# Performance work log

Hardware: AMD Instinct MI355X
Metric: run time of the kernel (lower is better)

Reference implementation:

```python
import jax, jax.numpy as jnp
import numpy as np

B, T, C = 8, 1024, 1024
H, D = 16, 64  # num_heads, head_size

def setup_inputs() -> dict:
    key = jax.random.key(0)
    ks = jax.random.split(key, 6)
    s = C ** -0.5
    return {
        "x": jax.random.normal(ks[0], (B, T, C), dtype=jnp.float32),
        "Wq": jax.random.normal(ks[1], (H, C, D), dtype=jnp.float32) * s,
        "Wk": jax.random.normal(ks[2], (H, C, D), dtype=jnp.float32) * s,
        "Wv": jax.random.normal(ks[3], (H, C, D), dtype=jnp.float32) * s,
        "Wproj": jax.random.normal(ks[4], (H * D, C), dtype=jnp.float32) * ((H * D) ** -0.5),
        "bproj": jnp.zeros((C,), dtype=jnp.float32),
    }

def reference(x, Wq, Wk, Wv, Wproj, bproj):
    # per-head QKV projections, batched over heads via einsum (same math as looped heads)
    q = jnp.einsum('btc,hcd->bhtd', x, Wq)
    k = jnp.einsum('btc,hcd->bhtd', x, Wk)
    v = jnp.einsum('btc,hcd->bhtd', x, Wv)
    scale = D ** -0.5  # k.shape[-1]**-0.5 in original head
    scores = jnp.einsum('bhtd,bhsd->bhts', q, k) * scale  # [B,H,T,T]
    Tn = x.shape[1]
    causal = jnp.tril(jnp.ones((Tn, Tn), dtype=bool))
    scores = jnp.where(causal, scores, jnp.float32(-jnp.inf))
    att = jax.nn.softmax(scores, axis=-1)
    out = jnp.einsum('bhts,bhsd->bhtd', att, v)          # [B,H,T,D]
    out = out.transpose(0, 2, 1, 3).reshape(x.shape[0], Tn, H * D)  # concat heads
    return out @ Wproj + bproj  # dropout is identity at p=0.0
```

## Files before the change

### kernel.cpp

```cpp
#include <hip/hip_runtime.h>
#include <hip/hip_bf16.h>

#define B_ 8
#define T_ 1024
#define C_ 1024
#define H_ 16
#define D_ 64
#define QKVLD 3072

typedef short v4s __attribute__((ext_vector_type(4)));
typedef short v8s __attribute__((ext_vector_type(8)));
typedef float v4f __attribute__((ext_vector_type(4)));
typedef float v16f __attribute__((ext_vector_type(16)));

__device__ __forceinline__ unsigned short f2b(float f) {
    unsigned int u = __builtin_bit_cast(unsigned int, f);
    unsigned int lsb = (u >> 16) & 1u;
    u += 0x7fffu + lsb;
    return (unsigned short)(u >> 16);
}

__device__ __forceinline__ v4s pack4(float p0, float p1, float p2, float p3) {
    unsigned int a = (__builtin_bit_cast(unsigned int, p0) + 0x8000u) >> 16;
    unsigned int b = (__builtin_bit_cast(unsigned int, p1) + 0x8000u) & 0xFFFF0000u;
    unsigned int c = (__builtin_bit_cast(unsigned int, p2) + 0x8000u) >> 16;
    unsigned int d = (__builtin_bit_cast(unsigned int, p3) + 0x8000u) & 0xFFFF0000u;
    union { unsigned int u[2]; v4s v; } t;
    t.u[0] = a | b; t.u[1] = c | d;
    return t.v;
}

#define MFMA32(A, B, C) __builtin_amdgcn_mfma_f32_16x16x32_bf16(A, B, C, 0, 0, 0)
#define MFMA16(A, B, C) __builtin_amdgcn_mfma_f32_16x16x16bf16_1k(A, B, C, 0, 0, 0)

#define GLOAD16(gp, lp)                                                          \
    __builtin_amdgcn_global_load_lds(                                            \
        (const __attribute__((address_space(1))) unsigned int*)(gp),             \
        (__attribute__((address_space(3))) unsigned int*)(lp), 16, 0, 0)

__global__ void prep_kernel(const float* __restrict__ x, const float* __restrict__ Wq,
                            const float* __restrict__ Wk, const float* __restrict__ Wv,
                            const float* __restrict__ Wproj,
                            unsigned short* __restrict__ xb,
                            unsigned short* __restrict__ WqkvT,
                            unsigned short* __restrict__ WprojT) {
    __shared__ unsigned short t[64][65];
    int g = blockIdx.x;
    if (g < 8192) {
        int i = (g * 256 + (int)threadIdx.x) * 4;
        float4 v = *(const float4*)(x + i);
        ushort4 o;
        o.x = f2b(v.x); o.y = f2b(v.y); o.z = f2b(v.z); o.w = f2b(v.w);
        *(ushort4*)(xb + i) = o;
    } else if (g < 8192 + 768) {
        int idx = g - 8192;
        int z = idx >> 4;
        int h = z / 3, part = z % 3;
        const float* src = (part == 0 ? Wq : (part == 1 ? Wk : Wv)) + (size_t)h * C_ * D_;
        int c0 = (idx & 15) * 64;
        for (int i = threadIdx.x; i < 4096; i += 256) {
            int r = i >> 6, d = i & 63;
            t[d][r] = f2b(src[(size_t)(c0 + r) * D_ + d]);
        }
        __syncthreads();
        unsigned short* dst = WqkvT + (size_t)(part * 1024 + h * 64) * C_;
        for (int i = threadIdx.x; i < 4096; i += 256) {
            int d = i >> 6, r = i & 63;
            dst[(size_t)d * C_ + c0 + r] = t[d][r];
        }
    } else {
        int idx = g - 8960;
        int n0 = (idx & 15) * 64, k0 = (idx >> 4) * 64;
        for (int i = threadIdx.x; i < 4096; i += 256) {
            int r = i >> 6, c = i & 63;
            t[c][r] = f2b(Wproj[(size_t)(k0 + r) * C_ + n0 + c]);
        }
        __syncthreads();
        for (int i = threadIdx.x; i < 4096; i += 256) {
            int n = i >> 6, k = i & 63;
            WprojT[(size_t)(n0 + n) * 1024 + k0 + k] = t[n][k];
        }
    }
}

__global__ __launch_bounds__(256, 2) void gemm_qk(const unsigned short* __restrict__ A,
                                                  const unsigned short* __restrict__ Bt,
                                                  unsigned short* __restrict__ Cout,
                                                  int M, int N, int K, int ldc) {
    constexpr int ABUF = 256 * 32;
    constexpr int BBUF = 128 * 32;
    __shared__ unsigned short smem[2 * ABUF + 2 * BBUF];
    unsigned short* lA0 = smem;
    unsigned short* lB0 = smem + 2 * ABUF;

    int tid = threadIdx.x;
    int m0 = blockIdx.y * 256, n0 = blockIdx.x * 128;
    int lane = tid & 63, w = tid >> 6;
    int half = lane >> 5, l32 = lane & 31;
    int wm = w >> 1, wn = w & 1;

    const unsigned short* gA[4];
    int offA[4];
    #pragma unroll
    for (int j = 0; j < 4; j++) {
        int c = j * 256 + tid;
        int row = c >> 2;
        int col8 = ((c & 3) ^ ((row >> 1) & 3)) * 8;
        gA[j] = A + (size_t)(m0 + row) * K + col8;
        offA[j] = (j * 256 + w * 64) * 16;
    }
    const unsigned short* gB[2];
    int offB[2];
    #pragma unroll
    for (int j = 0; j < 2; j++) {
        int c = j * 256 + tid;
        int row = c >> 2;
        int col8 = ((c & 3) ^ ((row >> 1) & 3)) * 8;
        gB[j] = Bt + (size_t)(n0 + row) * K + col8;
        offB[j] = (j * 256 + w * 64) * 16;
    }

    int am[4], bn[2];
    #pragma unroll
    for (int mi = 0; mi < 4; mi++) am[mi] = wm * 128 + mi * 32 + l32;
    #pragma unroll
    for (int ni = 0; ni < 2; ni++) bn[ni] = wn * 64 + ni * 32 + l32;

    v16f acc[4][2];
    #pragma unroll
    for (int mi = 0; mi < 4; mi++)
        #pragma unroll
        for (int ni = 0; ni < 2; ni++)
            #pragma unroll
            for (int r = 0; r < 16; r++) acc[mi][ni][r] = 0.f;

    int ktiles = K >> 5;
    #pragma unroll
    for (int j = 0; j < 4; j++) GLOAD16(gA[j], (char*)lA0 + offA[j]);
    #pragma unroll
    for (int j = 0; j < 2; j++) GLOAD16(gB[j], (char*)lB0 + offB[j]);

    for (int it = 0; it < ktiles; it++) {
        int cur = it & 1, nxt = cur ^ 1;
        __asm__ volatile("s_waitcnt vmcnt(0)" ::: "memory");
        __asm__ volatile("s_barrier" ::: "memory");
        {
            int kn = (it + 1 < ktiles) ? (it + 1) * 32 : it * 32;
            #pragma unroll
            for (int j = 0; j < 4; j++) GLOAD16(gA[j] + kn, (char*)(lA0 + nxt * ABUF) + offA[j]);
            #pragma unroll
            for (int j = 0; j < 2; j++) GLOAD16(gB[j] + kn, (char*)(lB0 + nxt * BBUF) + offB[j]);
        }
        const unsigned short* bufA = lA0 + cur * ABUF;
        const unsigned short* bufB = lB0 + cur * BBUF;
        #pragma unroll
        for (int step = 0; step < 2; step++) {
            int g = step * 2 + half;
            v8s af[4], bf[2];
            #pragma unroll
            for (int mi = 0; mi < 4; mi++)
                af[mi] = *(const v8s*)&bufA[am[mi] * 32 + ((g ^ ((am[mi] >> 1) & 3)) * 8)];
            #pragma unroll
            for (int ni = 0; ni < 2; ni++)
                bf[ni] = *(const v8s*)&bufB[bn[ni] * 32 + ((g ^ ((bn[ni] >> 1) & 3)) * 8)];
            #pragma unroll
            for (int mi = 0; mi < 4; mi++)
                #pragma unroll
                for (int ni = 0; ni < 2; ni++)
                    acc[mi][ni] = __builtin_amdgcn_mfma_f32_32x32x16_bf16(af[mi], bf[ni], acc[mi][ni], 0, 0, 0);
        }
    }
    float scl = (n0 >= 1024) ? 0.125f : 1.0f;
    #pragma unroll
    for (int mi = 0; mi < 4; mi++) {
        #pragma unroll
        for (int ni = 0; ni < 2; ni++) {
            int col = n0 + wn * 64 + ni * 32 + l32;
            #pragma unroll
            for (int r = 0; r < 16; r++) {
                int row = m0 + wm * 128 + mi * 32 + (r & 3) + 8 * (r >> 2) + 4 * half;
                Cout[(size_t)row * ldc + col] = f2b(acc[mi][ni][r] * scl);
            }
        }
    }
}

__global__ __launch_bounds__(256, 3) void gemm_v(const unsigned short* __restrict__ A,
                                                 const unsigned short* __restrict__ Bt,
                                                 unsigned short* __restrict__ Vt,
                                                 int M, int N, int K) {
    constexpr int ABUF = 128 * 32;
    constexpr int BBUF = 128 * 32;
    __shared__ unsigned short lA[3 * ABUF];
    __shared__ unsigned short lB[3 * BBUF];

    int tid = threadIdx.x;
    int lane = tid & 63, w = tid >> 6;
    int half = lane >> 5, l32 = lane & 31;
    int wm = w >> 1, wn = w & 1;

    int g = blockIdx.x;
    int nbm = M / 128;
    int stripe = nbm >> 3;
    int xcd = g & 7, s = g >> 3;
    int m0 = (xcd * stripe + (s % stripe)) * 128;
    int n0 = (s / stripe) * 128;

    const unsigned short* gA[2];
    int offA[2];
    #pragma unroll
    for (int j = 0; j < 2; j++) {
        int c = j * 256 + tid;
        int row = c >> 2;
        int col8 = ((c & 3) ^ ((row >> 1) & 3)) * 8;
        gA[j] = A + (size_t)(m0 + row) * K + col8;
        offA[j] = (j * 256 + w * 64) * 16;
    }
    const unsigned short* gB[2];
    int offB[2];
    #pragma unroll
    for (int j = 0; j < 2; j++) {
        int c = j * 256 + tid;
        int row = c >> 2;
        int col8 = ((c & 3) ^ ((row >> 1) & 3)) * 8;
        gB[j] = Bt + (size_t)(n0 + row) * K + col8;
        offB[j] = (j * 256 + w * 64) * 16;
    }

    int am[2], bn[2];
    #pragma unroll
    for (int mi = 0; mi < 2; mi++) am[mi] = wm * 64 + mi * 32 + l32;
    #pragma unroll
    for (int ni = 0; ni < 2; ni++) bn[ni] = wn * 64 + ni * 32 + l32;

    v16f acc[2][2];
    #pragma unroll
    for (int mi = 0; mi < 2; mi++)
        #pragma unroll
        for (int ni = 0; ni < 2; ni++)
            #pragma unroll
            for (int r = 0; r < 16; r++) acc[mi][ni][r] = 0.f;

    int kt = K >> 5;
    #pragma unroll
    for (int j = 0; j < 2; j++) GLOAD16(gA[j], (char*)lA + offA[j]);
    #pragma unroll
    for (int j = 0; j < 2; j++) GLOAD16(gB[j], (char*)lB + offB[j]);
    #pragma unroll
    for (int j = 0; j < 2; j++) GLOAD16(gA[j] + 32, (char*)(lA + ABUF) + offA[j]);
    #pragma unroll
    for (int j = 0; j < 2; j++) GLOAD16(gB[j] + 32, (char*)(lB + BBUF) + offB[j]);

    int cur = 0;
    for (int it = 0; it < kt; it++) {
        int nx2 = cur + 2; if (nx2 >= 3) nx2 -= 3;
        __asm__ volatile("s_waitcnt vmcnt(4)" ::: "memory");
        __asm__ volatile("s_barrier" ::: "memory");
        {
            int kn = ((it + 2 < kt) ? it + 2 : kt - 1) << 5;
            #pragma unroll
            for (int j = 0; j < 2; j++) GLOAD16(gA[j] + kn, (char*)(lA + nx2 * ABUF) + offA[j]);
            #pragma unroll
            for (int j = 0; j < 2; j++) GLOAD16(gB[j] + kn, (char*)(lB + nx2 * BBUF) + offB[j]);
        }
        const unsigned short* bufA = lA + cur * ABUF;
        const unsigned short* bufB = lB + cur * BBUF;
        #pragma unroll
        for (int step = 0; step < 2; step++) {
            int gch = step * 2 + half;
            v8s af[2], bf[2];
            #pragma unroll
            for (int mi = 0; mi < 2; mi++)
                af[mi] = *(const v8s*)&bufA[am[mi] * 32 + ((gch ^ ((am[mi] >> 1) & 3)) * 8)];
            #pragma unroll
            for (int ni = 0; ni < 2; ni++)
                bf[ni] = *(const v8s*)&bufB[bn[ni] * 32 + ((gch ^ ((bn[ni] >> 1) & 3)) * 8)];
            #pragma unroll
            for (int mi = 0; mi < 2; mi++)
                #pragma unroll
                for (int ni = 0; ni < 2; ni++)
                    acc[mi][ni] = __builtin_amdgcn_mfma_f32_32x32x16_bf16(af[mi], bf[ni], acc[mi][ni], 0, 0, 0);
        }
        cur = cur + 1; if (cur >= 3) cur -= 3;
    }
    unsigned short* sT = lA;
    int bB = m0 >> 10;
    int t0 = m0 & 1023;
    #pragma unroll
    for (int p = 0; p < 2; p++) {
        __syncthreads();
        if (wn == p) {
            #pragma unroll
            for (int mi = 0; mi < 2; mi++)
                #pragma unroll
                for (int ni = 0; ni < 2; ni++) {
                    int cl = ni * 32 + l32;
                    #pragma unroll
                    for (int r = 0; r < 16; r++) {
                        int rowl = wm * 64 + mi * 32 + (r & 3) + 8 * (r >> 2) + 4 * half;
                        sT[cl * 136 + rowl] = f2b(acc[mi][ni][r]);
                    }
                }
        }
        __syncthreads();
        #pragma unroll
        for (int j = 0; j < 4; j++) {
            int c = j * 256 + tid;
            int cl = c >> 4, ch = c & 15;
            int vcol = n0 + p * 64 + cl;
            int hh = vcol >> 6, dd = vcol & 63;
            *(v8s*)&Vt[(((size_t)bB * 16 + hh) * 64 + dd) * T_ + t0 + ch * 8] =
                *(const v8s*)&sT[cl * 136 + ch * 8];
        }
    }
}

__global__ __launch_bounds__(256, 3) void gemm_proj(const unsigned short* __restrict__ A,
                                                    const unsigned short* __restrict__ Bt,
                                                    float* __restrict__ Cout,
                                                    const float* __restrict__ bias,
                                                    int M, int N, int K) {
    constexpr int ABUF = 128 * 32;
    constexpr int BBUF = 128 * 32;
    __shared__ unsigned short lA[3 * ABUF];
    __shared__ unsigned short lB[3 * BBUF];

    int tid = threadIdx.x;
    int lane = tid & 63, w = tid >> 6;
    int half = lane >> 5, l32 = lane & 31;
    int wm = w >> 1, wn = w & 1;

    int g = blockIdx.x;
    int nbm = M / 128;
    int stripe = nbm >> 3;
    int xcd = g & 7, s = g >> 3;
    int m0 = (xcd * stripe + (s % stripe)) * 128;
    int n0 = (s / stripe) * 128;

    const unsigned short* gA[2];
    int offA[2];
    #pragma unroll
    for (int j = 0; j < 2; j++) {
        int c = j * 256 + tid;
        int row = c >> 2;
        int col8 = ((c & 3) ^ ((row >> 1) & 3)) * 8;
        gA[j] = A + (size_t)(m0 + row) * K + col8;
        offA[j] = (j * 256 + w * 64) * 16;
    }
    const unsigned short* gB[2];
    int offB[2];
    #pragma unroll
    for (int j = 0; j < 2; j++) {
        int c = j * 256 + tid;
        int row = c >> 2;
        int col8 = ((c & 3) ^ ((row >> 1) & 3)) * 8;
        gB[j] = Bt + (size_t)(n0 + row) * K + col8;
        offB[j] = (j * 256 + w * 64) * 16;
    }

    int am[2], bn[2];
    #pragma unroll
    for (int mi = 0; mi < 2; mi++) am[mi] = wm * 64 + mi * 32 + l32;
    #pragma unroll
    for (int ni = 0; ni < 2; ni++) bn[ni] = wn * 64 + ni * 32 + l32;

    v16f acc[2][2];
    #pragma unroll
    for (int mi = 0; mi < 2; mi++)
        #pragma unroll
        for (int ni = 0; ni < 2; ni++)
            #pragma unroll
            for (int r = 0; r < 16; r++) acc[mi][ni][r] = 0.f;

    int kt = K >> 5;
    #pragma unroll
    for (int j = 0; j < 2; j++) GLOAD16(gA[j], (char*)lA + offA[j]);
    #pragma unroll
    for (int j = 0; j < 2; j++) GLOAD16(gB[j], (char*)lB + offB[j]);
    #pragma unroll
    for (int j = 0; j < 2; j++) GLOAD16(gA[j] + 32, (char*)(lA + ABUF) + offA[j]);
    #pragma unroll
    for (int j = 0; j < 2; j++) GLOAD16(gB[j] + 32, (char*)(lB + BBUF) + offB[j]);

    int cur = 0;
    for (int it = 0; it < kt; it++) {
        int nx2 = cur + 2; if (nx2 >= 3) nx2 -= 3;
        __asm__ volatile("s_waitcnt vmcnt(4)" ::: "memory");
        __asm__ volatile("s_barrier" ::: "memory");
        {
            int kn = ((it + 2 < kt) ? it + 2 : kt - 1) << 5;
            #pragma unroll
            for (int j = 0; j < 2; j++) GLOAD16(gA[j] + kn, (char*)(lA + nx2 * ABUF) + offA[j]);
            #pragma unroll
            for (int j = 0; j < 2; j++) GLOAD16(gB[j] + kn, (char*)(lB + nx2 * BBUF) + offB[j]);
        }
        const unsigned short* bufA = lA + cur * ABUF;
        const unsigned short* bufB = lB + cur * BBUF;
        #pragma unroll
        for (int step = 0; step < 2; step++) {
            int gch = step * 2 + half;
            v8s af[2], bf[2];
            #pragma unroll
            for (int mi = 0; mi < 2; mi++)
                af[mi] = *(const v8s*)&bufA[am[mi] * 32 + ((gch ^ ((am[mi] >> 1) & 3)) * 8)];
            #pragma unroll
            for (int ni = 0; ni < 2; ni++)
                bf[ni] = *(const v8s*)&bufB[bn[ni] * 32 + ((gch ^ ((bn[ni] >> 1) & 3)) * 8)];
            #pragma unroll
            for (int mi = 0; mi < 2; mi++)
                #pragma unroll
                for (int ni = 0; ni < 2; ni++)
                    acc[mi][ni] = __builtin_amdgcn_mfma_f32_32x32x16_bf16(af[mi], bf[ni], acc[mi][ni], 0, 0, 0);
        }
        cur = cur + 1; if (cur >= 3) cur -= 3;
    }
    #pragma unroll
    for (int mi = 0; mi < 2; mi++) {
        #pragma unroll
        for (int ni = 0; ni < 2; ni++) {
            int col = n0 + wn * 64 + ni * 32 + l32;
            #pragma unroll
            for (int r = 0; r < 16; r++) {
                int row = m0 + wm * 64 + mi * 32 + (r & 3) + 8 * (r >> 2) + 4 * half;
                Cout[(size_t)row * N + col] = acc[mi][ni][r] + bias[col];
            }
        }
    }
}

__global__ __launch_bounds__(256) void attn_kernel(const unsigned short* __restrict__ QKV,
                                                   const unsigned short* __restrict__ Vt,
                                                   unsigned short* __restrict__ Ob) {
    int bh = blockIdx.x;
    int qt = 15 - blockIdx.y;
    int b = bh >> 4, h = bh & 15;
    int tid = threadIdx.x, lane = tid & 63, w = tid >> 6;
    int quad = lane >> 4, l16 = lane & 15;
    int qg0 = qt * 64 + w * 16;

    __shared__ unsigned short lK[2][2][64][32];
    __shared__ unsigned short lV[2][2][64][32];

    v8s aq0, aq1;
    {
        const unsigned short* qp = QKV + (size_t)(b * T_ + qg0 + l16) * QKVLD + h * 64;
        aq0 = *(const v8s*)(qp + quad * 8);
        aq1 = *(const v8s*)(qp + 32 + quad * 8);
    }

    const unsigned short* gK[2];
    const unsigned short* gV[2];
    int ldsOff[2];
    #pragma unroll
    for (int j = 0; j < 2; j++) {
        int c = j * 256 + tid;
        int halfp = c >> 8, row = (c >> 2) & 63;
        int col8 = ((c & 3) ^ ((row >> 1) & 3)) * 8;
        gK[j] = QKV + (size_t)(b * T_ + row) * QKVLD + 1024 + h * 64 + halfp * 32 + col8;
        gV[j] = Vt + ((size_t)bh * 64 + row) * T_ + halfp * 32 + col8;
        ldsOff[j] = (j * 256 + w * 64) * 16;
    }
    int rcol = (quad ^ ((l16 >> 1) & 3)) * 8;

    v4f accO[4];
    float lsum = 0.f;
    #pragma unroll
    for (int i = 0; i < 4; i++) accO[i] = (v4f){0.f, 0.f, 0.f, 0.f};

    int ntiles = qt + 1;

    #pragma unroll
    for (int j = 0; j < 2; j++) GLOAD16(gK[j], (char*)&lK[0][0][0][0] + ldsOff[j]);
    #pragma unroll
    for (int j = 0; j < 2; j++) GLOAD16(gV[j], (char*)&lV[0][0][0][0] + ldsOff[j]);

    for (int it = 0; it < ntiles; it++) {
        int cur = it & 1, nxt = cur ^ 1;
        int s0 = it * 64;
        __asm__ volatile("s_waitcnt vmcnt(0)" ::: "memory");
        __asm__ volatile("s_barrier" ::: "memory");
        {
            int itn = (it + 1 < ntiles) ? it + 1 : it;
            size_t koff = (size_t)itn * 64 * QKVLD;
            #pragma unroll
            for (int j = 0; j < 2; j++)
                GLOAD16(gK[j] + koff, (char*)&lK[nxt][0][0][0] + ldsOff[j]);
            size_t voff = (size_t)itn * 64;
            #pragma unroll
            for (int j = 0; j < 2; j++)
                GLOAD16(gV[j] + voff, (char*)&lV[nxt][0][0][0] + ldsOff[j]);
        }
        v4f sf[4];
        #pragma unroll
        for (int nt = 0; nt < 4; nt++) {
            v8s bk0 = *(const v8s*)&lK[cur][0][nt * 16 + l16][rcol];
            v8s bk1 = *(const v8s*)&lK[cur][1][nt * 16 + l16][rcol];
            v4f a = (v4f){0.f, 0.f, 0.f, 0.f};
            a = MFMA32(bk0, aq0, a);
            a = MFMA32(bk1, aq1, a);
            sf[nt] = a;
        }
        bool diag = (it == ntiles - 1);
        int qg = qg0 + l16;
        v4s pP[4];
        #pragma unroll
        for (int nt = 0; nt < 4; nt++) {
            float p[4];
            #pragma unroll
            for (int r = 0; r < 4; r++) {
                float e = __expf(sf[nt][r]);
                if (diag) {
                    int sg = s0 + nt * 16 + quad * 4 + r;
                    e = (sg > qg) ? 0.f : e;
                }
                p[r] = e;
                lsum += e;
            }
            pP[nt] = pack4(p[0], p[1], p[2], p[3]);
        }
        #pragma unroll
        for (int kb = 0; kb < 4; kb++) {
            int sc_ = kb >> 1;
            int ccg = (kb & 1) * 2 + (quad >> 1);
            #pragma unroll
            for (int dt = 0; dt < 4; dt++) {
                int d = dt * 16 + l16;
                int ccp = ccg ^ ((l16 >> 1) & 3);
                v4s bv = *(const v4s*)&lV[cur][sc_][d][ccp * 8 + (quad & 1) * 4];
                accO[dt] = MFMA16(pP[kb], bv, accO[dt]);
            }
        }
    }
    float ls = lsum;
    ls += __shfl_xor(ls, 16, 64);
    ls += __shfl_xor(ls, 32, 64);
    #pragma unroll
    for (int r = 0; r < 4; r++) {
        float lq = __shfl(ls, quad * 4 + r, 64);
        float inv = 1.0f / lq;
        int q = qg0 + quad * 4 + r;
        #pragma unroll
        for (int dt = 0; dt < 4; dt++) {
            int d = dt * 16 + l16;
            Ob[(size_t)(b * T_ + q) * (H_ * D_) + h * 64 + d] = f2b(accO[dt][r] * inv);
        }
    }
}

extern "C" void kernel_launch(void* const* d_in, const int* in_sizes, int n_in,
                              void* d_out, int out_size, void* d_ws, size_t ws_size,
                              hipStream_t stream) {
    const float* x     = (const float*)d_in[0];
    const float* Wq    = (const float*)d_in[1];
    const float* Wk    = (const float*)d_in[2];
    const float* Wv    = (const float*)d_in[3];
    const float* Wproj = (const float*)d_in[4];
    const float* bproj = (const float*)d_in[5];
    float* out = (float*)d_out;

    char* ws = (char*)d_ws;
    unsigned short* xb     = (unsigned short*)ws;
    unsigned short* WqkvT  = (unsigned short*)(ws + 16777216);
    unsigned short* WprojT = (unsigned short*)(ws + 23068672);
    unsigned short* QKV    = (unsigned short*)(ws + 25165824);
    unsigned short* Vt     = (unsigned short*)(ws + 75497472);
    unsigned short* Ob     = (unsigned short*)(ws + 92274688);

    prep_kernel<<<dim3(9216), dim3(256), 0, stream>>>(x, Wq, Wk, Wv, Wproj, xb, WqkvT, WprojT);
    gemm_qk<<<dim3(16, 32), dim3(256), 0, stream>>>(xb, WqkvT, QKV, 8192, 2048, 1024, QKVLD);
    gemm_v<<<dim3(512), dim3(256), 0, stream>>>(xb, WqkvT + (size_t)2048 * 1024, Vt, 8192, 1024, 1024);
    attn_kernel<<<dim3(128, 16), dim3(256), 0, stream>>>(QKV, Vt, Ob);
    gemm_proj<<<dim3(512), dim3(256), 0, stream>>>(Ob, WprojT, out, bproj, 8192, 1024, 1024);
}
```

Before: 235.7 us.

## Triple-buffer gemm_qk LDS pipeline and remap blocks by XCD for locality

The QK projection GEMM goes from double to triple LDS buffering, with global loads issued two K-tiles ahead. The wait drops from vmcnt(0) to vmcnt(6), so one tile's loads stay in flight while the current tile is computed. The 2D grid becomes a 1D grid of 512 blocks remapped so that each XCD (block id mod 8) handles a contiguous group of M-row tiles, which is meant to improve L2 reuse of A tiles. LDS use grows from 48KB to 72KB per block, which can lower occupancy below the launch-bounds target of 2 blocks per CU.

After: 238.0 us. About the same (+0.9%).

```diff
diff --git a/kernel.cpp b/kernel.cpp
--- a/kernel.cpp
+++ b/kernel.cpp
@@ -89,16 +89,19 @@
                                                   int M, int N, int K, int ldc) {
     constexpr int ABUF = 256 * 32;
     constexpr int BBUF = 128 * 32;
-    __shared__ unsigned short smem[2 * ABUF + 2 * BBUF];
-    unsigned short* lA0 = smem;
-    unsigned short* lB0 = smem + 2 * ABUF;
+    __shared__ unsigned short lA[3 * ABUF];
+    __shared__ unsigned short lB[3 * BBUF];
 
     int tid = threadIdx.x;
-    int m0 = blockIdx.y * 256, n0 = blockIdx.x * 128;
     int lane = tid & 63, w = tid >> 6;
     int half = lane >> 5, l32 = lane & 31;
     int wm = w >> 1, wn = w & 1;
 
+    int g = blockIdx.x;
+    int xcd = g & 7, s = g >> 3;
+    int m0 = (xcd * 4 + (s & 3)) * 256;
+    int n0 = (s >> 2) * 128;
+
     const unsigned short* gA[4];
     int offA[4];
     #pragma unroll
@@ -134,41 +137,47 @@
             #pragma unroll
             for (int r = 0; r < 16; r++) acc[mi][ni][r] = 0.f;
 
-    int ktiles = K >> 5;
-    #pragma unroll
-    for (int j = 0; j < 4; j++) GLOAD16(gA[j], (char*)lA0 + offA[j]);
-    #pragma unroll
-    for (int j = 0; j < 2; j++) GLOAD16(gB[j], (char*)lB0 + offB[j]);
-
-    for (int it = 0; it < ktiles; it++) {
-        int cur = it & 1, nxt = cur ^ 1;
-        __asm__ volatile("s_waitcnt vmcnt(0)" ::: "memory");
+    int kt = K >> 5;
+    #pragma unroll
+    for (int j = 0; j < 4; j++) GLOAD16(gA[j], (char*)lA + offA[j]);
+    #pragma unroll
+    for (int j = 0; j < 2; j++) GLOAD16(gB[j], (char*)lB + offB[j]);
+    #pragma unroll
+    for (int j = 0; j < 4; j++) GLOAD16(gA[j] + 32, (char*)(lA + ABUF) + offA[j]);
+    #pragma unroll
+    for (int j = 0; j < 2; j++) GLOAD16(gB[j] + 32, (char*)(lB + BBUF) + offB[j]);
+
+    int cur = 0;
+    for (int it = 0; it < kt; it++) {
+        int nx2 = cur + 2; if (nx2 >= 3) nx2 -= 3;
+        __asm__ volatile("s_waitcnt vmcnt(6)" ::: "memory");
         __asm__ volatile("s_barrier" ::: "memory");
         {
-            int kn = (it + 1 < ktiles) ? (it + 1) * 32 : it * 32;
-            #pragma unroll
-            for (int j = 0; j < 4; j++) GLOAD16(gA[j] + kn, (char*)(lA0 + nxt * ABUF) + offA[j]);
-            #pragma unroll
-            for (int j = 0; j < 2; j++) GLOAD16(gB[j] + kn, (char*)(lB0 + nxt * BBUF) + offB[j]);
-        }
-        const unsigned short* bufA = lA0 + cur * ABUF;
-        const unsigned short* bufB = lB0 + cur * BBUF;
+            int kn = ((it + 2 < kt) ? it + 2 : kt - 1) << 5;
+            #pragma unroll
+            for (int j = 0; j < 4; j++) GLOAD16(gA[j] + kn, (char*)(lA + nx2 * ABUF) + offA[j]);
+            #pragma unroll
+            for (int j = 0; j < 2; j++) GLOAD16(gB[j] + kn, (char*)(lB + nx2 * BBUF) + offB[j]);
+        }
+        const unsigned short* bufA = lA + cur * ABUF;
+        const unsigned short* bufB = lB + cur * BBUF;
         #pragma unroll
         for (int step = 0; step < 2; step++) {
-            int g = step * 2 + half;
+            int gc = step * 2 + half;
             v8s af[4], bf[2];
             #pragma unroll
             for (int mi = 0; mi < 4; mi++)
-                af[mi] = *(const v8s*)&bufA[am[mi] * 32 + ((g ^ ((am[mi] >> 1) & 3)) * 8)];
+                af[mi] = *(const v8s*)&bufA[am[mi] * 32 + ((gc ^ ((am[mi] >> 1) & 3)) * 8)];
             #pragma unroll
             for (int ni = 0; ni < 2; ni++)
-                bf[ni] = *(const v8s*)&bufB[bn[ni] * 32 + ((g ^ ((bn[ni] >> 1) & 3)) * 8)];
+                bf[ni] = *(const v8s*)&bufB[bn[ni] * 32 + ((gc ^ ((bn[ni] >> 1) & 3)) * 8)];
             #pragma unroll
             for (int mi = 0; mi < 4; mi++)
                 #pragma unroll
                 for (int ni = 0; ni < 2; ni++)
                     acc[mi][ni] = __builtin_amdgcn_mfma_f32_32x32x16_bf16(af[mi], bf[ni], acc[mi][ni], 0, 0, 0);
         }
+        cur = cur + 1; if (cur >= 3) cur -= 3;
     }
     float scl = (n0 >= 1024) ? 0.125f : 1.0f;
     #pragma unroll
@@ -567,7 +576,7 @@
     unsigned short* Ob     = (unsigned short*)(ws + 92274688);
 
     prep_kernel<<<dim3(9216), dim3(256), 0, stream>>>(x, Wq, Wk, Wv, Wproj, xb, WqkvT, WprojT);
-    gemm_qk<<<dim3(16, 32), dim3(256), 0, stream>>>(xb, WqkvT, QKV, 8192, 2048, 1024, QKVLD);
+    gemm_qk<<<dim3(512), dim3(256), 0, stream>>>(xb, WqkvT, QKV, 8192, 2048, 1024, QKVLD);
     gemm_v<<<dim3(512), dim3(256), 0, stream>>>(xb, WqkvT + (size_t)2048 * 1024, Vt, 8192, 1024, 1024);
     attn_kernel<<<dim3(128, 16), dim3(256), 0, stream>>>(QKV, Vt, Ob);
     gemm_proj<<<dim3(512), dim3(256), 0, stream>>>(Ob, WprojT, out, bproj, 8192, 1024, 1024);
```

## Fuse Q/K and V projection GEMMs into one launch with branchy epilogue

Applied to the files above, without the earlier changes.

Merges the separate QK and V projection GEMM kernels into a single 256x128-tile kernel over the full 3072-column QKV weight. Blocks whose columns fall in the V range write a transposed V layout through shared memory, and the others write row-major Q/K with scaling. This removes one kernel launch and the tail between the two GEMMs, giving a single larger grid. In exchange the V part now uses the 2-wave/CU tile config instead of its tuned 3-stage 128x128 kernel, and the transpose staging needs larger shared-memory strides.

Result: no change. 235.6 us (-0.1%).

```diff
diff --git a/kernel.cpp b/kernel.cpp
--- a/kernel.cpp
+++ b/kernel.cpp
@@ -83,10 +83,11 @@
     }
 }
 
-__global__ __launch_bounds__(256, 2) void gemm_qk(const unsigned short* __restrict__ A,
-                                                  const unsigned short* __restrict__ Bt,
-                                                  unsigned short* __restrict__ Cout,
-                                                  int M, int N, int K, int ldc) {
+__global__ __launch_bounds__(256, 2) void gemm_qkv(const unsigned short* __restrict__ A,
+                                                   const unsigned short* __restrict__ Bt,
+                                                   unsigned short* __restrict__ Cout,
+                                                   unsigned short* __restrict__ Vt,
+                                                   int M, int N, int K, int ldc) {
     constexpr int ABUF = 256 * 32;
     constexpr int BBUF = 128 * 32;
     __shared__ unsigned short smem[2 * ABUF + 2 * BBUF];
@@ -155,14 +156,14 @@
         const unsigned short* bufB = lB0 + cur * BBUF;
         #pragma unroll
         for (int step = 0; step < 2; step++) {
-            int g = step * 2 + half;
+            int gc = step * 2 + half;
             v8s af[4], bf[2];
             #pragma unroll
             for (int mi = 0; mi < 4; mi++)
-                af[mi] = *(const v8s*)&bufA[am[mi] * 32 + ((g ^ ((am[mi] >> 1) & 3)) * 8)];
+                af[mi] = *(const v8s*)&bufA[am[mi] * 32 + ((gc ^ ((am[mi] >> 1) & 3)) * 8)];
             #pragma unroll
             for (int ni = 0; ni < 2; ni++)
-                bf[ni] = *(const v8s*)&bufB[bn[ni] * 32 + ((g ^ ((bn[ni] >> 1) & 3)) * 8)];
+                bf[ni] = *(const v8s*)&bufB[bn[ni] * 32 + ((gc ^ ((bn[ni] >> 1) & 3)) * 8)];
             #pragma unroll
             for (int mi = 0; mi < 4; mi++)
                 #pragma unroll
@@ -170,147 +171,51 @@
                     acc[mi][ni] = __builtin_amdgcn_mfma_f32_32x32x16_bf16(af[mi], bf[ni], acc[mi][ni], 0, 0, 0);
         }
     }
-    float scl = (n0 >= 1024) ? 0.125f : 1.0f;
-    #pragma unroll
-    for (int mi = 0; mi < 4; mi++) {
-        #pragma unroll
-        for (int ni = 0; ni < 2; ni++) {
-            int col = n0 + wn * 64 + ni * 32 + l32;
-            #pragma unroll
-            for (int r = 0; r < 16; r++) {
-                int row = m0 + wm * 128 + mi * 32 + (r & 3) + 8 * (r >> 2) + 4 * half;
-                Cout[(size_t)row * ldc + col] = f2b(acc[mi][ni][r] * scl);
-            }
-        }
-    }
-}
-
-__global__ __launch_bounds__(256, 3) void gemm_v(const unsigned short* __restrict__ A,
-                                                 const unsigned short* __restrict__ Bt,
-                                                 unsigned short* __restrict__ Vt,
-                                                 int M, int N, int K) {
-    constexpr int ABUF = 128 * 32;
-    constexpr int BBUF = 128 * 32;
-    __shared__ unsigned short lA[3 * ABUF];
-    __shared__ unsigned short lB[3 * BBUF];
-
-    int tid = threadIdx.x;
-    int lane = tid & 63, w = tid >> 6;
-    int half = lane >> 5, l32 = lane & 31;
-    int wm = w >> 1, wn = w & 1;
-
-    int g = blockIdx.x;
-    int nbm = M / 128;
-    int stripe = nbm >> 3;
-    int xcd = g & 7, s = g >> 3;
-    int m0 = (xcd * stripe + (s % stripe)) * 128;
-    int n0 = (s / stripe) * 128;
-
-    const unsigned short* gA[2];
-    int offA[2];
-    #pragma unroll
-    for (int j = 0; j < 2; j++) {
-        int c = j * 256 + tid;
-        int row = c >> 2;
-        int col8 = ((c & 3) ^ ((row >> 1) & 3)) * 8;
-        gA[j] = A + (size_t)(m0 + row) * K + col8;
-        offA[j] = (j * 256 + w * 64) * 16;
-    }
-    const unsigned short* gB[2];
-    int offB[2];
-    #pragma unroll
-    for (int j = 0; j < 2; j++) {
-        int c = j * 256 + tid;
-        int row = c >> 2;
-        int col8 = ((c & 3) ^ ((row >> 1) & 3)) * 8;
-        gB[j] = Bt + (size_t)(n0 + row) * K + col8;
-        offB[j] = (j * 256 + w * 64) * 16;
-    }
-
-    int am[2], bn[2];
-    #pragma unroll
-    for (int mi = 0; mi < 2; mi++) am[mi] = wm * 64 + mi * 32 + l32;
-    #pragma unroll
-    for (int ni = 0; ni < 2; ni++) bn[ni] = wn * 64 + ni * 32 + l32;
-
-    v16f acc[2][2];
-    #pragma unroll
-    for (int mi = 0; mi < 2; mi++)
-        #pragma unroll
-        for (int ni = 0; ni < 2; ni++)
-            #pragma unroll
-            for (int r = 0; r < 16; r++) acc[mi][ni][r] = 0.f;
-
-    int kt = K >> 5;
-    #pragma unroll
-    for (int j = 0; j < 2; j++) GLOAD16(gA[j], (char*)lA + offA[j]);
-    #pragma unroll
-    for (int j = 0; j < 2; j++) GLOAD16(gB[j], (char*)lB + offB[j]);
-    #pragma unroll
-    for (int j = 0; j < 2; j++) GLOAD16(gA[j] + 32, (char*)(lA + ABUF) + offA[j]);
-    #pragma unroll
-    for (int j = 0; j < 2; j++) GLOAD16(gB[j] + 32, (char*)(lB + BBUF) + offB[j]);
-
-    int cur = 0;
-    for (int it = 0; it < kt; it++) {
-        int nx2 = cur + 2; if (nx2 >= 3) nx2 -= 3;
-        __asm__ volatile("s_waitcnt vmcnt(4)" ::: "memory");
-        __asm__ volatile("s_barrier" ::: "memory");
-        {
-            int kn = ((it + 2 < kt) ? it + 2 : kt - 1) << 5;
-            #pragma unroll
-            for (int j = 0; j < 2; j++) GLOAD16(gA[j] + kn, (char*)(lA + nx2 * ABUF) + offA[j]);
-            #pragma unroll
-            for (int j = 0; j < 2; j++) GLOAD16(gB[j] + kn, (char*)(lB + nx2 * BBUF) + offB[j]);
-        }
-        const unsigned short* bufA = lA + cur * ABUF;
-        const unsigned short* bufB = lB + cur * BBUF;
-        #pragma unroll
-        for (int step = 0; step < 2; step++) {
-            int gch = step * 2 + half;
-            v8s af[2], bf[2];
-            #pragma unroll
-            for (int mi = 0; mi < 2; mi++)
-                af[mi] = *(const v8s*)&bufA[am[mi] * 32 + ((gch ^ ((am[mi] >> 1) & 3)) * 8)];
-            #pragma unroll
-            for (int ni = 0; ni < 2; ni++)
-                bf[ni] = *(const v8s*)&bufB[bn[ni] * 32 + ((gch ^ ((bn[ni] >> 1) & 3)) * 8)];
-            #pragma unroll
-            for (int mi = 0; mi < 2; mi++)
+
+    if (n0 < 2048) {
+        float scl = (n0 >= 1024) ? 0.125f : 1.0f;
+        #pragma unroll
+        for (int mi = 0; mi < 4; mi++) {
+            #pragma unroll
+            for (int ni = 0; ni < 2; ni++) {
+                int col = n0 + wn * 64 + ni * 32 + l32;
                 #pragma unroll
-                for (int ni = 0; ni < 2; ni++)
-                    acc[mi][ni] = __builtin_amdgcn_mfma_f32_32x32x16_bf16(af[mi], bf[ni], acc[mi][ni], 0, 0, 0);
-        }
-        cur = cur + 1; if (cur >= 3) cur -= 3;
-    }
-    unsigned short* sT = lA;
-    int bB = m0 >> 10;
-    int t0 = m0 & 1023;
-    #pragma unroll
-    for (int p = 0; p < 2; p++) {
-        __syncthreads();
-        if (wn == p) {
-            #pragma unroll
-            for (int mi = 0; mi < 2; mi++)
+                for (int r = 0; r < 16; r++) {
+                    int row = m0 + wm * 128 + mi * 32 + (r & 3) + 8 * (r >> 2) + 4 * half;
+                    Cout[(size_t)row * ldc + col] = f2b(acc[mi][ni][r] * scl);
+                }
+            }
+        }
+    } else {
+        unsigned short* sT = smem;
+        int bB = m0 >> 10;
+        int t0 = m0 & 1023;
+        #pragma unroll
+        for (int p = 0; p < 2; p++) {
+            __syncthreads();
+            if (wn == p) {
                 #pragma unroll
-                for (int ni = 0; ni < 2; ni++) {
-                    int cl = ni * 32 + l32;
+                for (int mi = 0; mi < 4; mi++)
                     #pragma unroll
-                    for (int r = 0; r < 16; r++) {
-                        int rowl = wm * 64 + mi * 32 + (r & 3) + 8 * (r >> 2) + 4 * half;
-                        sT[cl * 136 + rowl] = f2b(acc[mi][ni][r]);
+                    for (int ni = 0; ni < 2; ni++) {
+                        int cl = ni * 32 + l32;
+                        #pragma unroll
+                        for (int r = 0; r < 16; r++) {
+                            int rowl = wm * 128 + mi * 32 + (r & 3) + 8 * (r >> 2) + 4 * half;
+                            sT[cl * 264 + rowl] = f2b(acc[mi][ni][r]);
+                        }
                     }
-                }
-        }
-        __syncthreads();
-        #pragma unroll
-        for (int j = 0; j < 4; j++) {
-            int c = j * 256 + tid;
-            int cl = c >> 4, ch = c & 15;
-            int vcol = n0 + p * 64 + cl;
-            int hh = vcol >> 6, dd = vcol & 63;
-            *(v8s*)&Vt[(((size_t)bB * 16 + hh) * 64 + dd) * T_ + t0 + ch * 8] =
-                *(const v8s*)&sT[cl * 136 + ch * 8];
+            }
+            __syncthreads();
+            #pragma unroll
+            for (int j = 0; j < 8; j++) {
+                int c = j * 256 + tid;
+                int cl = c >> 5, ch = c & 31;
+                int vcol = (n0 - 2048) + p * 64 + cl;
+                int hh = vcol >> 6, dd = vcol & 63;
+                *(v8s*)&Vt[(((size_t)bB * 16 + hh) * 64 + dd) * T_ + t0 + ch * 8] =
+                    *(const v8s*)&sT[cl * 264 + ch * 8];
+            }
         }
     }
 }
@@ -567,8 +472,7 @@
     unsigned short* Ob     = (unsigned short*)(ws + 92274688);
 
     prep_kernel<<<dim3(9216), dim3(256), 0, stream>>>(x, Wq, Wk, Wv, Wproj, xb, WqkvT, WprojT);
-    gemm_qk<<<dim3(16, 32), dim3(256), 0, stream>>>(xb, WqkvT, QKV, 8192, 2048, 1024, QKVLD);
-    gemm_v<<<dim3(512), dim3(256), 0, stream>>>(xb, WqkvT + (size_t)2048 * 1024, Vt, 8192, 1024, 1024);
+    gemm_qkv<<<dim3(24, 32), dim3(256), 0, stream>>>(xb, WqkvT, QKV, Vt, 8192, 3072, 1024, QKVLD);
     attn_kernel<<<dim3(128, 16), dim3(256), 0, stream>>>(QKV, Vt, Ob);
     gemm_proj<<<dim3(512), dim3(256), 0, stream>>>(Ob, WprojT, out, bproj, 8192, 1024, 1024);
 }
```
